# Kernel tuning notes

Measured on AMD Instinct MI355X. Metric: run time of the kernel, lower is better.

The kernel has to match this reference:

```python
import jax, jax.numpy as jnp
import numpy as np

EMB_DIM = 384
HEAD_DIM = 64
B, T = 512, 256


def setup_inputs() -> dict:
    key = jax.random.key(0)
    k1, k2, k3, k4 = jax.random.split(key, 4)
    inputs = jax.random.normal(k1, (B, T, EMB_DIM), dtype=jnp.float32)
    # torch nn.Linear weight layout: [out_features, in_features]
    s = EMB_DIM ** -0.5
    WQ = jax.random.normal(k2, (HEAD_DIM, EMB_DIM), dtype=jnp.float32) * s
    WK = jax.random.normal(k3, (HEAD_DIM, EMB_DIM), dtype=jnp.float32) * s
    WV = jax.random.normal(k4, (HEAD_DIM, EMB_DIM), dtype=jnp.float32) * s
    return {"inputs": inputs, "WQ": WQ, "WK": WK, "WV": WV}


def reference(inputs, WQ, WK, WV):
    # Linear (no bias): x @ W.T
    q = jnp.einsum('btc,dc->btd', inputs, WQ)  # [B,T,D]
    k = jnp.einsum('btc,dc->btd', inputs, WK)
    v = jnp.einsum('btc,dc->btd', inputs, WV)
    scale = k.shape[-1] ** -0.5
    scores = jnp.einsum('bqd,bkd->bqk', q, k) * scale  # [B,T,T]
    Tq = inputs.shape[1]
    causal = jnp.tril(jnp.ones((Tq, Tq), dtype=bool))
    scores = jnp.where(causal, scores, -jnp.inf)
    weights = jax.nn.softmax(scores, axis=-1)
    # dropout omitted (eval mode) for a deterministic reference
    out = jnp.einsum('bqk,bkd->bqd', weights, v)  # [B,T,D]
    return out
```

## Files before the change

kernel.cpp:

```cpp
#include <hip/hip_runtime.h>


typedef short s16x8 __attribute__((ext_vector_type(8)));
typedef float f32x4 __attribute__((ext_vector_type(4)));
typedef unsigned short u16;
typedef unsigned short u16x4 __attribute__((ext_vector_type(4)));

__device__ __forceinline__ u16 f2bf(float f) {
  unsigned u = __builtin_bit_cast(unsigned, f);
  u = (u + 0x7fffu + ((u >> 16) & 1u)) >> 16;
  return (u16)u;
}

__device__ __forceinline__ s16x8 pack8(float4 a, float4 b) {
  s16x8 h;
  h[0] = (short)f2bf(a.x); h[1] = (short)f2bf(a.y);
  h[2] = (short)f2bf(a.z); h[3] = (short)f2bf(a.w);
  h[4] = (short)f2bf(b.x); h[5] = (short)f2bf(b.y);
  h[6] = (short)f2bf(b.z); h[7] = (short)f2bf(b.w);
  return h;
}

#define MFMA16 __builtin_amdgcn_mfma_f32_16x16x32_bf16

#define XC(b) ((b) * 16384)
#define WC(b) (32768 + (b) * 12288)
#define QS 57344
#define KS 90112
#define VS 122880

__global__ __launch_bounds__(1024) void head_kernel(
    const float* __restrict__ x,
    const float* __restrict__ WQ, const float* __restrict__ WK,
    const float* __restrict__ WV, float* __restrict__ out)
{
  __shared__ char smem[155648];
  const int tid = threadIdx.x;
  const int l  = tid & 63;
  const int w  = tid >> 6;
  const int g  = l >> 4, li = l & 15;
  const long xbase = (long)blockIdx.x * (256 * 384);
  const long obase = (long)blockIdx.x * (256 * 64);

  const int srow  = tid >> 2;
  const int sslot = tid & 3;
  const bool do_w = (tid < 768);
  const float* wrp = nullptr;
  if (do_w)
    wrp = (srow < 64) ? (WQ + srow * 384)
         : (srow < 128) ? (WK + (srow - 64) * 384)
                        : (WV + (srow - 128) * 384);
  const int wswz = (srow >> 1) & 3;
  const int rswz = (li >> 1) & 3;

  {
    const float* px = x + xbase + srow * 384 + sslot * 8;
    float4 xa = *reinterpret_cast<const float4*>(px);
    float4 xb = *reinterpret_cast<const float4*>(px + 4);
    *reinterpret_cast<s16x8*>(smem + XC(0) + srow * 64 + ((sslot ^ wswz) << 4)) =
        pack8(xa, xb);
    if (do_w) {
      float4 wa = *reinterpret_cast<const float4*>(wrp + sslot * 8);
      float4 wb = *reinterpret_cast<const float4*>(wrp + sslot * 8 + 4);
      *reinterpret_cast<s16x8*>(smem + WC(0) + srow * 64 + ((sslot ^ wswz) << 4)) =
          pack8(wa, wb);
    }
  }
  __syncthreads();

  f32x4 acc[12];
#pragma unroll
  for (int nt = 0; nt < 12; ++nt) acc[nt] = (f32x4){0.f, 0.f, 0.f, 0.f};

#pragma unroll 1
  for (int t = 0; t < 12; ++t) {
    float4 xa, xb, wa, wb;
    if (t < 11) {
      const float* px = x + xbase + srow * 384 + (t + 1) * 32 + sslot * 8;
      xa = *reinterpret_cast<const float4*>(px);
      xb = *reinterpret_cast<const float4*>(px + 4);
      if (do_w) {
        wa = *reinterpret_cast<const float4*>(wrp + (t + 1) * 32 + sslot * 8);
        wb = *reinterpret_cast<const float4*>(wrp + (t + 1) * 32 + sslot * 8 + 4);
      }
    }
    const int cb = t & 1;
    s16x8 bf = *reinterpret_cast<const s16x8*>(
        smem + XC(cb) + (16 * w + li) * 64 + ((g ^ rswz) << 4));
#pragma unroll
    for (int h = 0; h < 3; ++h) {
      s16x8 af[4];
#pragma unroll
      for (int j = 0; j < 4; ++j)
        af[j] = *reinterpret_cast<const s16x8*>(
            smem + WC(cb) + ((h * 4 + j) * 16 + li) * 64 + ((g ^ rswz) << 4));
#pragma unroll
      for (int j = 0; j < 4; ++j)
        acc[h * 4 + j] = MFMA16(af[j], bf, acc[h * 4 + j], 0, 0, 0);
    }
    if (t < 11) {
      *reinterpret_cast<s16x8*>(
          smem + XC(cb ^ 1) + srow * 64 + ((sslot ^ wswz) << 4)) = pack8(xa, xb);
      if (do_w)
        *reinterpret_cast<s16x8*>(
            smem + WC(cb ^ 1) + srow * 64 + ((sslot ^ wswz) << 4)) = pack8(wa, wb);
    }
    __syncthreads();
  }

  {
    const int row = 16 * w + li;
#pragma unroll
    for (int nt = 0; nt < 8; ++nt) {
      const int b0 = (nt < 4) ? QS : KS;
      const int slot = (nt & 3) * 2 + (g >> 1);
      u16x4 pk;
      pk[0] = f2bf(acc[nt][0]); pk[1] = f2bf(acc[nt][1]);
      pk[2] = f2bf(acc[nt][2]); pk[3] = f2bf(acc[nt][3]);
      *reinterpret_cast<u16x4*>(
          smem + b0 + row * 128 + ((slot ^ (row & 7)) << 4) + (g & 1) * 8) = pk;
    }
#pragma unroll
    for (int nt = 8; nt < 12; ++nt)
#pragma unroll
      for (int r = 0; r < 4; ++r) {
        int d = (nt - 8) * 16 + g * 4 + r;
        *reinterpret_cast<u16*>(
            smem + VS + d * 512 + ((row * 2) ^ ((d & 7) << 4))) = f2bf(acc[nt][r]);
      }
  }
  __syncthreads();

  char* Pw = smem + w * 2048;
  const int qt = w;
  s16x8 qf[2];
#pragma unroll
  for (int dk = 0; dk < 2; ++dk) {
    int row = qt * 16 + li;
    qf[dk] = *reinterpret_cast<const s16x8*>(
        smem + QS + row * 128 + (((dk * 4 + g) ^ (row & 7)) << 4));
  }

  f32x4 o[4];
  float m[4], lsum[4];
#pragma unroll
  for (int r = 0; r < 4; ++r) { m[r] = -1e30f; lsum[r] = 0.f; }
#pragma unroll
  for (int nd = 0; nd < 4; ++nd) o[nd] = (f32x4){0.f, 0.f, 0.f, 0.f};

  const int nc = (qt >> 2) + 1;
#pragma unroll 1
  for (int c = 0; c < nc; ++c) {
    f32x4 s[4];
#pragma unroll
    for (int nj = 0; nj < 4; ++nj) s[nj] = (f32x4){0.f, 0.f, 0.f, 0.f};
#pragma unroll
    for (int dk = 0; dk < 2; ++dk) {
#pragma unroll
      for (int nj = 0; nj < 4; ++nj) {
        int rb = c * 64 + nj * 16 + li;
        s16x8 kf = *reinterpret_cast<const s16x8*>(
            smem + KS + rb * 128 + (((dk * 4 + g) ^ (rb & 7)) << 4));
        s[nj] = MFMA16(qf[dk], kf, s[nj], 0, 0, 0);
      }
    }
    const bool last = (c == nc - 1);
#pragma unroll
    for (int nj = 0; nj < 4; ++nj)
#pragma unroll
      for (int r = 0; r < 4; ++r) {
        float v = s[nj][r] * 0.125f;
        if (last && (c * 64 + nj * 16 + li) > (qt * 16 + g * 4 + r)) v = -1e30f;
        s[nj][r] = v;
      }
    float alpha[4];
#pragma unroll
    for (int r = 0; r < 4; ++r) {
      float pm = fmaxf(fmaxf(s[0][r], s[1][r]), fmaxf(s[2][r], s[3][r]));
      pm = fmaxf(pm, __shfl_xor(pm, 1));
      pm = fmaxf(pm, __shfl_xor(pm, 2));
      pm = fmaxf(pm, __shfl_xor(pm, 4));
      pm = fmaxf(pm, __shfl_xor(pm, 8));
      float mn = fmaxf(m[r], pm);
      alpha[r] = __expf(m[r] - mn);
      m[r] = mn;
    }
    float psum[4] = {0.f, 0.f, 0.f, 0.f};
#pragma unroll
    for (int nj = 0; nj < 4; ++nj)
#pragma unroll
      for (int r = 0; r < 4; ++r) {
        float p = __expf(s[nj][r] - m[r]);
        psum[r] += p;
        int rowp = g * 4 + r;
        *reinterpret_cast<u16*>(
            Pw + rowp * 128 + ((nj * 32 + li * 2) ^ ((rowp & 7) << 4))) = f2bf(p);
      }
#pragma unroll
    for (int r = 0; r < 4; ++r) {
      float ps = psum[r];
      ps += __shfl_xor(ps, 1);
      ps += __shfl_xor(ps, 2);
      ps += __shfl_xor(ps, 4);
      ps += __shfl_xor(ps, 8);
      lsum[r] = lsum[r] * alpha[r] + ps;
    }
#pragma unroll
    for (int nd = 0; nd < 4; ++nd)
#pragma unroll
      for (int r = 0; r < 4; ++r) o[nd][r] *= alpha[r];

    __asm__ volatile("s_waitcnt lgkmcnt(0)" ::: "memory");
    s16x8 pa[2];
#pragma unroll
    for (int kk = 0; kk < 2; ++kk)
      pa[kk] = *reinterpret_cast<const s16x8*>(
          Pw + li * 128 + (((kk * 4 + g) ^ (li & 7)) << 4));
#pragma unroll
    for (int nd = 0; nd < 4; ++nd) {
#pragma unroll
      for (int kk = 0; kk < 2; ++kk) {
        int d = nd * 16 + li;
        s16x8 vf = *reinterpret_cast<const s16x8*>(
            smem + VS + d * 512 + ((c * 128 + kk * 64 + g * 16) ^ ((d & 7) << 4)));
        o[nd] = MFMA16(pa[kk], vf, o[nd], 0, 0, 0);
      }
    }
  }
#pragma unroll
  for (int r = 0; r < 4; ++r) lsum[r] = 1.f / lsum[r];
#pragma unroll
  for (int nd = 0; nd < 4; ++nd)
#pragma unroll
    for (int r = 0; r < 4; ++r)
      out[obase + (qt * 16 + g * 4 + r) * 64 + nd * 16 + li] = o[nd][r] * lsum[r];
}

extern "C" void kernel_launch(void* const* d_in, const int* in_sizes, int n_in,
                              void* d_out, int out_size, void* d_ws, size_t ws_size,
                              hipStream_t stream) {
  const float* x  = (const float*)d_in[0];
  const float* WQ = (const float*)d_in[1];
  const float* WK = (const float*)d_in[2];
  const float* WV = (const float*)d_in[3];
  float* out = (float*)d_out;

  head_kernel<<<dim3(512), dim3(1024), 0, stream>>>(x, WQ, WK, WV, out);
}
```

Before: 62.43 us.

## Retile QKV projection as 4x3 MFMA blocks per wave and use hardware bf16 conversion

```diff
diff --git a/kernel.cpp b/kernel.cpp
--- a/kernel.cpp
+++ b/kernel.cpp
@@ -3,22 +3,25 @@
 
 typedef short s16x8 __attribute__((ext_vector_type(8)));
 typedef float f32x4 __attribute__((ext_vector_type(4)));
+typedef float f32x2 __attribute__((ext_vector_type(2)));
+typedef unsigned int u32;
+typedef unsigned int u32x4 __attribute__((ext_vector_type(4)));
 typedef unsigned short u16;
 typedef unsigned short u16x4 __attribute__((ext_vector_type(4)));
-
+typedef __bf16 bf16x2 __attribute__((ext_vector_type(2)));
+
+__device__ __forceinline__ u32 cvt2(float x, float y) {
+  f32x2 v = {x, y};
+  bf16x2 b = __builtin_convertvector(v, bf16x2);
+  return __builtin_bit_cast(u32, b);
+}
 __device__ __forceinline__ u16 f2bf(float f) {
-  unsigned u = __builtin_bit_cast(unsigned, f);
-  u = (u + 0x7fffu + ((u >> 16) & 1u)) >> 16;
-  return (u16)u;
-}
-
+  __bf16 b = (__bf16)f;
+  return __builtin_bit_cast(u16, b);
+}
 __device__ __forceinline__ s16x8 pack8(float4 a, float4 b) {
-  s16x8 h;
-  h[0] = (short)f2bf(a.x); h[1] = (short)f2bf(a.y);
-  h[2] = (short)f2bf(a.z); h[3] = (short)f2bf(a.w);
-  h[4] = (short)f2bf(b.x); h[5] = (short)f2bf(b.y);
-  h[6] = (short)f2bf(b.z); h[7] = (short)f2bf(b.w);
-  return h;
+  u32x4 p = {cvt2(a.x, a.y), cvt2(a.z, a.w), cvt2(b.x, b.y), cvt2(b.z, b.w)};
+  return __builtin_bit_cast(s16x8, p);
 }
 
 #define MFMA16 __builtin_amdgcn_mfma_f32_16x16x32_bf16
@@ -39,6 +42,7 @@
   const int l  = tid & 63;
   const int w  = tid >> 6;
   const int g  = l >> 4, li = l & 15;
+  const int wr = w >> 2, wc = w & 3;
   const long xbase = (long)blockIdx.x * (256 * 384);
   const long obase = (long)blockIdx.x * (256 * 64);
 
@@ -68,9 +72,12 @@
   }
   __syncthreads();
 
-  f32x4 acc[12];
-#pragma unroll
-  for (int nt = 0; nt < 12; ++nt) acc[nt] = (f32x4){0.f, 0.f, 0.f, 0.f};
+  f32x4 acc[4][3];
+#pragma unroll
+  for (int bi = 0; bi < 4; ++bi)
+#pragma unroll
+    for (int ai = 0; ai < 3; ++ai)
+      acc[bi][ai] = (f32x4){0.f, 0.f, 0.f, 0.f};
 
 #pragma unroll 1
   for (int t = 0; t < 12; ++t) {
@@ -85,19 +92,22 @@
       }
     }
     const int cb = t & 1;
-    s16x8 bf = *reinterpret_cast<const s16x8*>(
-        smem + XC(cb) + (16 * w + li) * 64 + ((g ^ rswz) << 4));
-#pragma unroll
-    for (int h = 0; h < 3; ++h) {
-      s16x8 af[4];
-#pragma unroll
-      for (int j = 0; j < 4; ++j)
-        af[j] = *reinterpret_cast<const s16x8*>(
-            smem + WC(cb) + ((h * 4 + j) * 16 + li) * 64 + ((g ^ rswz) << 4));
-#pragma unroll
-      for (int j = 0; j < 4; ++j)
-        acc[h * 4 + j] = MFMA16(af[j], bf, acc[h * 4 + j], 0, 0, 0);
-    }
+    s16x8 bf[4];
+#pragma unroll
+    for (int bi = 0; bi < 4; ++bi)
+      bf[bi] = *reinterpret_cast<const s16x8*>(
+          smem + XC(cb) + (wr * 64 + bi * 16 + li) * 64 + ((g ^ rswz) << 4));
+    s16x8 af[3];
+#pragma unroll
+    for (int ai = 0; ai < 3; ++ai)
+      af[ai] = *reinterpret_cast<const s16x8*>(
+          smem + WC(cb) + (wc * 48 + ai * 16 + li) * 64 + ((g ^ rswz) << 4));
+#pragma unroll
+    for (int bi = 0; bi < 4; ++bi)
+#pragma unroll
+      for (int ai = 0; ai < 3; ++ai)
+        acc[bi][ai] = MFMA16(af[ai], bf[bi], acc[bi][ai], 0, 0, 0);
+
     if (t < 11) {
       *reinterpret_cast<s16x8*>(
           smem + XC(cb ^ 1) + srow * 64 + ((sslot ^ wswz) << 4)) = pack8(xa, xb);
@@ -108,26 +118,31 @@
     __syncthreads();
   }
 
-  {
-    const int row = 16 * w + li;
-#pragma unroll
-    for (int nt = 0; nt < 8; ++nt) {
-      const int b0 = (nt < 4) ? QS : KS;
-      const int slot = (nt & 3) * 2 + (g >> 1);
-      u16x4 pk;
-      pk[0] = f2bf(acc[nt][0]); pk[1] = f2bf(acc[nt][1]);
-      pk[2] = f2bf(acc[nt][2]); pk[3] = f2bf(acc[nt][3]);
-      *reinterpret_cast<u16x4*>(
-          smem + b0 + row * 128 + ((slot ^ (row & 7)) << 4) + (g & 1) * 8) = pk;
-    }
-#pragma unroll
-    for (int nt = 8; nt < 12; ++nt)
-#pragma unroll
-      for (int r = 0; r < 4; ++r) {
-        int d = (nt - 8) * 16 + g * 4 + r;
-        *reinterpret_cast<u16*>(
-            smem + VS + d * 512 + ((row * 2) ^ ((d & 7) << 4))) = f2bf(acc[nt][r]);
-      }
+#pragma unroll
+  for (int bi = 0; bi < 4; ++bi) {
+    const int row = wr * 64 + bi * 16 + li;
+#pragma unroll
+    for (int ai = 0; ai < 3; ++ai) {
+      const int nb = wc * 48 + ai * 16;
+      if (nb < 128) {
+        const int b0 = (nb < 64) ? QS : KS;
+        const int d16 = nb & 63;
+        const int slot = (d16 >> 3) + (g >> 1);
+        u16x4 pk;
+        pk[0] = f2bf(acc[bi][ai][0]); pk[1] = f2bf(acc[bi][ai][1]);
+        pk[2] = f2bf(acc[bi][ai][2]); pk[3] = f2bf(acc[bi][ai][3]);
+        *reinterpret_cast<u16x4*>(
+            smem + b0 + row * 128 + ((slot ^ (row & 7)) << 4) + (g & 1) * 8) = pk;
+      } else {
+#pragma unroll
+        for (int r = 0; r < 4; ++r) {
+          int d = nb - 128 + g * 4 + r;
+          *reinterpret_cast<u16*>(
+              smem + VS + d * 512 + ((row * 2) ^ ((d & 7) << 4))) =
+              f2bf(acc[bi][ai][r]);
+        }
+      }
+    }
   }
   __syncthreads();
 
```

Result: no change. 62.01 us (-0.7%).
